# Kernel tuning notes

Hardware: AMD Instinct MI355X
Metric: run time of the kernel (lower is better)

The kernel has to match this reference:

```python
import jax, jax.numpy as jnp
import numpy as np

LOG2PI = 1.8378770664093453  # log(2*pi)


def _pixel_positions(d, h, w):
    # centered coordinates, stacked as (x, y, z) per the torch module
    z = jnp.arange(d, dtype=jnp.float32) - (d - 1) / 2.0
    y = jnp.arange(h, dtype=jnp.float32) - (h - 1) / 2.0
    x = jnp.arange(w, dtype=jnp.float32) - (w - 1) / 2.0
    zz = jnp.broadcast_to(z[:, None, None], (d, h, w))
    yy = jnp.broadcast_to(y[None, :, None], (d, h, w))
    xx = jnp.broadcast_to(x[None, None, :], (d, h, w))
    return jnp.stack([xx, yy, zz], axis=-1).reshape(-1, 3)  # (N, 3)


def setup_inputs() -> dict:
    key = jax.random.key(0)
    k0, k1, k2, k3, k4 = jax.random.split(key, 5)
    B, D = 512, 256
    d, h, w = 16, 64, 64
    scale = 1.0 / np.sqrt(D)
    return {
        "representation": jax.random.normal(k0, (B, D), dtype=jnp.float32),
        "mean_w": jax.random.normal(k1, (3, D), dtype=jnp.float32) * scale,
        "mean_b": jax.random.normal(k2, (3,), dtype=jnp.float32) * 0.1,
        "scale_w": jax.random.normal(k3, (6, D), dtype=jnp.float32) * scale,
        "scale_b": jax.random.normal(k4, (6,), dtype=jnp.float32) * 0.1,
        "pixel_positions": _pixel_positions(d, h, w),
    }


def reference(representation, mean_w, mean_b, scale_w, scale_b, pixel_positions):
    # linear heads
    means = representation @ mean_w.T + mean_b            # (B, 3)
    s_raw = representation @ scale_w.T + scale_b          # (B, 6)
    s = jax.nn.elu(s_raw) + 1.0                           # (B, 6)

    # FillScaleTriL with SoftplusTransform on the diagonal.
    # tril_indices(3,3) row-major order: (0,0),(1,0),(1,1),(2,0),(2,1),(2,2)
    l00 = jax.nn.softplus(s[:, 0])
    l10 = s[:, 1]
    l11 = jax.nn.softplus(s[:, 2])
    l20 = s[:, 3]
    l21 = s[:, 4]
    l22 = jax.nn.softplus(s[:, 5])

    # Mahalanobis term via analytic forward-substitution of L z = (x - mu)
    diff = pixel_positions[None, :, :] - means[:, None, :]  # (B, N, 3)
    z0 = diff[..., 0] / l00[:, None]
    z1 = (diff[..., 1] - l10[:, None] * z0) / l11[:, None]
    z2 = (diff[..., 2] - l20[:, None] * z0 - l21[:, None] * z1) / l22[:, None]
    maha = z0 * z0 + z1 * z1 + z2 * z2                     # (B, N)

    log_det = jnp.log(l00) + jnp.log(l11) + jnp.log(l22)   # (B,)
    log_probs = -0.5 * maha - 1.5 * LOG2PI - log_det[:, None]  # (B, N)

    # stable normalize over the pixel grid (matches torch code incl. eps)
    lp = log_probs - jnp.max(log_probs, axis=1, keepdims=True)
    p = jnp.exp(lp)
    return p / (jnp.sum(p, axis=1, keepdims=True) + 1e-10)
```

## Files before the change

### kernel.cpp

```cpp
#include <hip/hip_runtime.h>
#include <math.h>


#define LOG2PI_F 1.8378770664093453f

__device__ __forceinline__ float waveMax(float v) {
#pragma unroll
    for (int off = 32; off; off >>= 1) v = fmaxf(v, __shfl_xor(v, off, 64));
    return v;
}
__device__ __forceinline__ float waveSum(float v) {
#pragma unroll
    for (int off = 32; off; off >>= 1) v += __shfl_xor(v, off, 64);
    return v;
}

__global__ __launch_bounds__(1024, 8)
void mvn_profile_kernel(const float* __restrict__ rep,
                        const float* __restrict__ mean_w,
                        const float* __restrict__ mean_b,
                        const float* __restrict__ scale_w,
                        const float* __restrict__ scale_b,
                        float* __restrict__ out)
{
    const int b    = blockIdx.x;
    const int tid  = threadIdx.x;
    const int lane = tid & 63;
    const int wave = tid >> 6;

    __shared__ float s_dots[9];
    __shared__ float s_params[10];
    __shared__ float s_red[16];
    __shared__ float s_bc[2];

    if (wave < 9) {
        const float4* r4 = (const float4*)(rep + (size_t)b * 256);
        const float*  wrow = (wave < 3) ? (mean_w + wave * 256)
                                        : (scale_w + (wave - 3) * 256);
        const float4* w4 = (const float4*)wrow;
        float4 a = r4[lane];
        float4 w = w4[lane];
        float d = a.x * w.x + a.y * w.y + a.z * w.z + a.w * w.w;
        d = waveSum(d);
        if (lane == 0) s_dots[wave] = d;
    }
    __syncthreads();

    if (tid == 0) {
        float mx = s_dots[0] + mean_b[0];
        float my = s_dots[1] + mean_b[1];
        float mz = s_dots[2] + mean_b[2];
        float s[6];
#pragma unroll
        for (int j = 0; j < 6; j++) {
            float x = s_dots[3 + j] + scale_b[j];
            s[j] = (x > 0.0f) ? (x + 1.0f) : (expm1f(x) + 1.0f);
        }
        float l00 = fmaxf(s[0], 0.0f) + log1pf(expf(-fabsf(s[0])));
        float l10 = s[1];
        float l11 = fmaxf(s[2], 0.0f) + log1pf(expf(-fabsf(s[2])));
        float l20 = s[3];
        float l21 = s[4];
        float l22 = fmaxf(s[5], 0.0f) + log1pf(expf(-fabsf(s[5])));
        s_params[0] = mx;
        s_params[1] = my;
        s_params[2] = mz;
        s_params[3] = 1.0f / l00;
        s_params[4] = l10;
        s_params[5] = 1.0f / l11;
        s_params[6] = l20;
        s_params[7] = l21;
        s_params[8] = 1.0f / l22;
        s_params[9] = -1.5f * LOG2PI_F - (logf(l00) + logf(l11) + logf(l22));
    }
    __syncthreads();

    const float mx  = s_params[0], my  = s_params[1], mz  = s_params[2];
    const float i00 = s_params[3], l10 = s_params[4], i11 = s_params[5];
    const float l20 = s_params[6], l21 = s_params[7], i22 = s_params[8];
    const float cb  = s_params[9];

    const float py = (float)(tid >> 4) - 31.5f;
    const float dy = py - my;

    float cc[4];
    float e2[4];
    float tmax = -INFINITY;
#pragma unroll
    for (int j = 0; j < 4; j++) {
        float px = (float)(((tid * 4) & 63) + j) - 31.5f;
        float dx = px - mx;
        float z0 = dx * i00;
        float z1 = (dy - l10 * z0) * i11;
        float c2 = mz + l20 * z0 + l21 * z1;
        e2[j] = c2 * i22;
        cc[j] = cb - 0.5f * (z0 * z0 + z1 * z1);
        float kf = rintf(c2 + 7.5f);
        kf = fminf(fmaxf(kf, 0.0f), 15.0f);
        float t  = (kf - 7.5f) * i22;
        float z2 = t - e2[j];
        tmax = fmaxf(tmax, cc[j] - 0.5f * (z2 * z2));
    }

    tmax = waveMax(tmax);
    if (lane == 0) s_red[wave] = tmax;
    __syncthreads();
    if (wave == 0) {
        float v = (lane < 16) ? s_red[lane] : -INFINITY;
        v = waveMax(v);
        if (lane == 0) s_bc[0] = v;
    }
    __syncthreads();
    const float m = s_bc[0];

    float ce[4];
#pragma unroll
    for (int j = 0; j < 4; j++) ce[j] = cc[j] - m;

    float tsum = 0.0f;
#pragma unroll
    for (int k = 0; k < 16; k++) {
        float t = ((float)k - 7.5f) * i22;
#pragma unroll
        for (int j = 0; j < 4; j++) {
            float z2 = t - e2[j];
            tsum += __expf(ce[j] - 0.5f * (z2 * z2));
        }
    }
    tsum = waveSum(tsum);
    if (lane == 0) s_red[wave] = tsum;
    __syncthreads();
    if (wave == 0) {
        float v = (lane < 16) ? s_red[lane] : 0.0f;
        v = waveSum(v);
        if (lane == 0) s_bc[1] = 1.0f / (v + 1e-10f);
    }
    __syncthreads();
    const float r = s_bc[1];

    float* orow = out + (size_t)b * 65536 + (size_t)tid * 4;
#pragma unroll
    for (int k = 0; k < 16; k++) {
        float t = ((float)k - 7.5f) * i22;
        float z20 = t - e2[0];
        float z21 = t - e2[1];
        float z22 = t - e2[2];
        float z23 = t - e2[3];
        float4 o;
        o.x = __expf(ce[0] - 0.5f * (z20 * z20)) * r;
        o.y = __expf(ce[1] - 0.5f * (z21 * z21)) * r;
        o.z = __expf(ce[2] - 0.5f * (z22 * z22)) * r;
        o.w = __expf(ce[3] - 0.5f * (z23 * z23)) * r;
        *(float4*)(orow + (size_t)k * 4096) = o;
    }
}

extern "C" void kernel_launch(void* const* d_in, const int* in_sizes, int n_in,
                              void* d_out, int out_size, void* d_ws, size_t ws_size,
                              hipStream_t stream) {
    const float* rep     = (const float*)d_in[0];
    const float* mean_w  = (const float*)d_in[1];
    const float* mean_b  = (const float*)d_in[2];
    const float* scale_w = (const float*)d_in[3];
    const float* scale_b = (const float*)d_in[4];
    float* out = (float*)d_out;

    const int B = in_sizes[0] / 256;
    hipLaunchKernelGGL(mvn_profile_kernel, dim3(B), dim3(1024), 0, stream,
                       rep, mean_w, mean_b, scale_w, scale_b, out);
}
```

Before: 178.5 us.

## Split into param/sum kernel and wide store kernel, drop max pass

Removes the max-subtraction pass, since the constant shift cancels in the normalization, and drops the log-det constant. Splits the work into a per-batch kernel that computes parameters and the normalizing sum into workspace, and a second kernel over 8x more blocks that writes the output. The goal is more parallelism and latency hiding on the large output write, plus fewer block-level reductions and barriers. The cost is a second launch and recomputing the exponentials, and skipping the max shift risks underflow when the peak density is very small.

New measurement: 154.6 us. -13.4%, faster.

```diff
diff --git a/kernel.cpp b/kernel.cpp
--- a/kernel.cpp
+++ b/kernel.cpp
@@ -2,26 +2,24 @@
 #include <math.h>
 
 
-#define LOG2PI_F 1.8378770664093453f
-
+__device__ __forceinline__ float waveSum(float v) {
+#pragma unroll
+    for (int off = 32; off; off >>= 1) v += __shfl_xor(v, off, 64);
+    return v;
+}
 __device__ __forceinline__ float waveMax(float v) {
 #pragma unroll
     for (int off = 32; off; off >>= 1) v = fmaxf(v, __shfl_xor(v, off, 64));
     return v;
 }
-__device__ __forceinline__ float waveSum(float v) {
-#pragma unroll
-    for (int off = 32; off; off >>= 1) v += __shfl_xor(v, off, 64);
-    return v;
-}
 
 __global__ __launch_bounds__(1024, 8)
-void mvn_profile_kernel(const float* __restrict__ rep,
-                        const float* __restrict__ mean_w,
-                        const float* __restrict__ mean_b,
-                        const float* __restrict__ scale_w,
-                        const float* __restrict__ scale_b,
-                        float* __restrict__ out)
+void mvn_params_sum_kernel(const float* __restrict__ rep,
+                           const float* __restrict__ mean_w,
+                           const float* __restrict__ mean_b,
+                           const float* __restrict__ scale_w,
+                           const float* __restrict__ scale_b,
+                           float* __restrict__ ws)
 {
     const int b    = blockIdx.x;
     const int tid  = threadIdx.x;
@@ -29,9 +27,161 @@
     const int wave = tid >> 6;
 
     __shared__ float s_dots[9];
-    __shared__ float s_params[10];
+    __shared__ float s_params[9];
     __shared__ float s_red[16];
-    __shared__ float s_bc[2];
+
+    if (wave < 9) {
+        const float4* r4 = (const float4*)(rep + (size_t)b * 256);
+        const float*  wrow = (wave < 3) ? (mean_w + wave * 256)
+                                        : (scale_w + (wave - 3) * 256);
+        const float4* w4 = (const float4*)wrow;
+        float4 a = r4[lane];
+        float4 w = w4[lane];
+        float d = a.x * w.x + a.y * w.y + a.z * w.z + a.w * w.w;
+        d = waveSum(d);
+        if (lane == 0) s_dots[wave] = d;
+    }
+    __syncthreads();
+
+    if (tid == 0) {
+        float mx = s_dots[0] + mean_b[0];
+        float my = s_dots[1] + mean_b[1];
+        float mz = s_dots[2] + mean_b[2];
+        float s[6];
+#pragma unroll
+        for (int j = 0; j < 6; j++) {
+            float x = s_dots[3 + j] + scale_b[j];
+            s[j] = (x > 0.0f) ? (x + 1.0f) : (expm1f(x) + 1.0f);
+        }
+        float l00 = fmaxf(s[0], 0.0f) + log1pf(expf(-fabsf(s[0])));
+        float l10 = s[1];
+        float l11 = fmaxf(s[2], 0.0f) + log1pf(expf(-fabsf(s[2])));
+        float l20 = s[3];
+        float l21 = s[4];
+        float l22 = fmaxf(s[5], 0.0f) + log1pf(expf(-fabsf(s[5])));
+        float p0 = mx, p1 = my, p2 = mz;
+        float p3 = 1.0f / l00, p4 = l10, p5 = 1.0f / l11;
+        float p6 = l20, p7 = l21, p8 = 1.0f / l22;
+        s_params[0] = p0; s_params[1] = p1; s_params[2] = p2;
+        s_params[3] = p3; s_params[4] = p4; s_params[5] = p5;
+        s_params[6] = p6; s_params[7] = p7; s_params[8] = p8;
+        float* wrow = ws + (size_t)b * 16;
+        wrow[0] = p0; wrow[1] = p1; wrow[2] = p2;
+        wrow[3] = p3; wrow[4] = p4; wrow[5] = p5;
+        wrow[6] = p6; wrow[7] = p7; wrow[8] = p8;
+    }
+    __syncthreads();
+
+    const float mx  = s_params[0], my  = s_params[1], mz  = s_params[2];
+    const float i00 = s_params[3], l10 = s_params[4], i11 = s_params[5];
+    const float l20 = s_params[6], l21 = s_params[7], i22 = s_params[8];
+
+    const float py = (float)(tid >> 4) - 31.5f;
+    const float dy = py - my;
+
+    float qn[4];
+    float e2[4];
+#pragma unroll
+    for (int j = 0; j < 4; j++) {
+        float px = (float)(((tid * 4) & 63) + j) - 31.5f;
+        float dx = px - mx;
+        float z0 = dx * i00;
+        float z1 = (dy - l10 * z0) * i11;
+        e2[j] = (mz + l20 * z0 + l21 * z1) * i22;
+        qn[j] = -0.5f * (z0 * z0 + z1 * z1);
+    }
+
+    float tsum = 0.0f;
+#pragma unroll
+    for (int k = 0; k < 16; k++) {
+        float t = ((float)k - 7.5f) * i22;
+#pragma unroll
+        for (int j = 0; j < 4; j++) {
+            float z2 = t - e2[j];
+            tsum += __expf(qn[j] - 0.5f * z2 * z2);
+        }
+    }
+    tsum = waveSum(tsum);
+    if (lane == 0) s_red[wave] = tsum;
+    __syncthreads();
+    if (wave == 0) {
+        float v = (lane < 16) ? s_red[lane] : 0.0f;
+        v = waveSum(v);
+        if (lane == 0) ws[(size_t)b * 16 + 9] = 1.0f / (v + 1e-10f);
+    }
+}
+
+__global__ __launch_bounds__(512, 8)
+void mvn_store_kernel(const float* __restrict__ ws,
+                      float* __restrict__ out)
+{
+    const int g   = blockIdx.x;
+    const int b   = g >> 3;
+    const int k0  = (g & 7) << 1;
+    const int tid = threadIdx.x;
+
+    const float* __restrict__ P = ws + (size_t)b * 16;
+    const float mx  = P[0], my  = P[1], mz  = P[2];
+    const float i00 = P[3], l10 = P[4], i11 = P[5];
+    const float l20 = P[6], l21 = P[7], i22 = P[8];
+    const float r   = P[9];
+
+    float qn[2][4], e2[2][4];
+#pragma unroll
+    for (int i = 0; i < 2; i++) {
+        int c4 = tid + 512 * i;
+        float py = (float)(c4 >> 4) - 31.5f;
+        float dy = py - my;
+#pragma unroll
+        for (int j = 0; j < 4; j++) {
+            float px = (float)(((c4 * 4) & 63) + j) - 31.5f;
+            float dx = px - mx;
+            float z0 = dx * i00;
+            float z1 = (dy - l10 * z0) * i11;
+            e2[i][j] = (mz + l20 * z0 + l21 * z1) * i22;
+            qn[i][j] = -0.5f * (z0 * z0 + z1 * z1);
+        }
+    }
+
+    float* orow = out + (size_t)b * 65536;
+#pragma unroll
+    for (int kk = 0; kk < 2; kk++) {
+        int k = k0 + kk;
+        float t = ((float)k - 7.5f) * i22;
+#pragma unroll
+        for (int i = 0; i < 2; i++) {
+            int c4 = tid + 512 * i;
+            float z20 = t - e2[i][0];
+            float z21 = t - e2[i][1];
+            float z22 = t - e2[i][2];
+            float z23 = t - e2[i][3];
+            float4 o;
+            o.x = __expf(qn[i][0] - 0.5f * z20 * z20) * r;
+            o.y = __expf(qn[i][1] - 0.5f * z21 * z21) * r;
+            o.z = __expf(qn[i][2] - 0.5f * z22 * z22) * r;
+            o.w = __expf(qn[i][3] - 0.5f * z23 * z23) * r;
+            *(float4*)(orow + (size_t)k * 4096 + (size_t)c4 * 4) = o;
+        }
+    }
+}
+
+__global__ __launch_bounds__(1024, 8)
+void mvn_profile_fallback(const float* __restrict__ rep,
+                          const float* __restrict__ mean_w,
+                          const float* __restrict__ mean_b,
+                          const float* __restrict__ scale_w,
+                          const float* __restrict__ scale_b,
+                          float* __restrict__ out)
+{
+    const int b    = blockIdx.x;
+    const int tid  = threadIdx.x;
+    const int lane = tid & 63;
+    const int wave = tid >> 6;
+
+    __shared__ float s_dots[9];
+    __shared__ float s_params[9];
+    __shared__ float s_red[16];
+    __shared__ float s_bc;
 
     if (wave < 9) {
         const float4* r4 = (const float4*)(rep + (size_t)b * 256);
@@ -71,51 +221,26 @@
         s_params[6] = l20;
         s_params[7] = l21;
         s_params[8] = 1.0f / l22;
-        s_params[9] = -1.5f * LOG2PI_F - (logf(l00) + logf(l11) + logf(l22));
     }
     __syncthreads();
 
     const float mx  = s_params[0], my  = s_params[1], mz  = s_params[2];
     const float i00 = s_params[3], l10 = s_params[4], i11 = s_params[5];
     const float l20 = s_params[6], l21 = s_params[7], i22 = s_params[8];
-    const float cb  = s_params[9];
 
     const float py = (float)(tid >> 4) - 31.5f;
     const float dy = py - my;
 
-    float cc[4];
-    float e2[4];
-    float tmax = -INFINITY;
+    float qn[4], e2[4];
 #pragma unroll
     for (int j = 0; j < 4; j++) {
         float px = (float)(((tid * 4) & 63) + j) - 31.5f;
         float dx = px - mx;
         float z0 = dx * i00;
         float z1 = (dy - l10 * z0) * i11;
-        float c2 = mz + l20 * z0 + l21 * z1;
-        e2[j] = c2 * i22;
-        cc[j] = cb - 0.5f * (z0 * z0 + z1 * z1);
-        float kf = rintf(c2 + 7.5f);
-        kf = fminf(fmaxf(kf, 0.0f), 15.0f);
-        float t  = (kf - 7.5f) * i22;
-        float z2 = t - e2[j];
-        tmax = fmaxf(tmax, cc[j] - 0.5f * (z2 * z2));
-    }
-
-    tmax = waveMax(tmax);
-    if (lane == 0) s_red[wave] = tmax;
-    __syncthreads();
-    if (wave == 0) {
-        float v = (lane < 16) ? s_red[lane] : -INFINITY;
-        v = waveMax(v);
-        if (lane == 0) s_bc[0] = v;
-    }
-    __syncthreads();
-    const float m = s_bc[0];
-
-    float ce[4];
-#pragma unroll
-    for (int j = 0; j < 4; j++) ce[j] = cc[j] - m;
+        e2[j] = (mz + l20 * z0 + l21 * z1) * i22;
+        qn[j] = -0.5f * (z0 * z0 + z1 * z1);
+    }
 
     float tsum = 0.0f;
 #pragma unroll
@@ -124,7 +249,7 @@
 #pragma unroll
         for (int j = 0; j < 4; j++) {
             float z2 = t - e2[j];
-            tsum += __expf(ce[j] - 0.5f * (z2 * z2));
+            tsum += __expf(qn[j] - 0.5f * z2 * z2);
         }
     }
     tsum = waveSum(tsum);
@@ -133,10 +258,10 @@
     if (wave == 0) {
         float v = (lane < 16) ? s_red[lane] : 0.0f;
         v = waveSum(v);
-        if (lane == 0) s_bc[1] = 1.0f / (v + 1e-10f);
-    }
-    __syncthreads();
-    const float r = s_bc[1];
+        if (lane == 0) s_bc = 1.0f / (v + 1e-10f);
+    }
+    __syncthreads();
+    const float r = s_bc;
 
     float* orow = out + (size_t)b * 65536 + (size_t)tid * 4;
 #pragma unroll
@@ -147,10 +272,10 @@
         float z22 = t - e2[2];
         float z23 = t - e2[3];
         float4 o;
-        o.x = __expf(ce[0] - 0.5f * (z20 * z20)) * r;
-        o.y = __expf(ce[1] - 0.5f * (z21 * z21)) * r;
-        o.z = __expf(ce[2] - 0.5f * (z22 * z22)) * r;
-        o.w = __expf(ce[3] - 0.5f * (z23 * z23)) * r;
+        o.x = __expf(qn[0] - 0.5f * z20 * z20) * r;
+        o.y = __expf(qn[1] - 0.5f * z21 * z21) * r;
+        o.z = __expf(qn[2] - 0.5f * z22 * z22) * r;
+        o.w = __expf(qn[3] - 0.5f * z23 * z23) * r;
         *(float4*)(orow + (size_t)k * 4096) = o;
     }
 }
@@ -166,6 +291,14 @@
     float* out = (float*)d_out;
 
     const int B = in_sizes[0] / 256;
-    hipLaunchKernelGGL(mvn_profile_kernel, dim3(B), dim3(1024), 0, stream,
-                       rep, mean_w, mean_b, scale_w, scale_b, out);
-}
+
+    if (ws_size >= (size_t)B * 16 * sizeof(float)) {
+        hipLaunchKernelGGL(mvn_params_sum_kernel, dim3(B), dim3(1024), 0, stream,
+                           rep, mean_w, mean_b, scale_w, scale_b, (float*)d_ws);
+        hipLaunchKernelGGL(mvn_store_kernel, dim3(B * 8), dim3(512), 0, stream,
+                           (const float*)d_ws, out);
+    } else {
+        hipLaunchKernelGGL(mvn_profile_fallback, dim3(B), dim3(1024), 0, stream,
+                           rep, mean_w, mean_b, scale_w, scale_b, out);
+    }
+}
```
